# Performance work log

Measured on AMD Instinct MI355X. Metric: run time of the kernel, lower is better.

## Reference

```python
import jax, jax.numpy as jnp
import numpy as np

BN_EPS = 1e-5

def _batchnorm(h, gamma, beta):
    # PyTorch BatchNorm1d in training mode: biased batch statistics over dim 0
    mu = jnp.mean(h, axis=0)
    var = jnp.mean((h - mu) ** 2, axis=0)
    return (h - mu) * jax.lax.rsqrt(var + BN_EPS) * gamma + beta


def setup_inputs() -> dict:
    key = jax.random.key(0)
    ks = jax.random.split(key, 8)
    N, E, D = 50000, 800000, 128
    x = jax.random.normal(ks[0], (N, D), dtype=jnp.float32)
    edge_index = jax.random.randint(ks[1], (2, E), 0, N, dtype=jnp.int64)
    s1 = 1.0 / np.sqrt(D)
    W1 = jax.random.uniform(ks[2], (D, D), jnp.float32, -s1, s1)
    b1 = jax.random.uniform(ks[3], (D,), jnp.float32, -s1, s1)
    W2 = jax.random.uniform(ks[4], (D, D), jnp.float32, -s1, s1)
    b2 = jax.random.uniform(ks[5], (D,), jnp.float32, -s1, s1)
    g1 = jnp.ones((D,), jnp.float32); beta1 = jnp.zeros((D,), jnp.float32)
    g2 = jnp.ones((D,), jnp.float32); beta2 = jnp.zeros((D,), jnp.float32)
    eps = jnp.array([0.1], jnp.float32)
    return {"x": x, "edge_index": edge_index, "eps": eps,
            "W1": W1, "b1": b1, "g1": g1, "beta1": beta1,
            "W2": W2, "b2": b2, "g2": g2, "beta2": beta2}


def reference(x, edge_index, eps, W1, b1, g1, beta1, W2, b2, g2, beta2):
    src, dst = edge_index[0], edge_index[1]
    N = x.shape[0]
    # gather by src, scatter-add to dst
    aggr = jax.ops.segment_sum(x[src], dst, num_segments=N)
    out = (1.0 + eps) * x + aggr  # eps broadcast (shape [1])
    h = jax.nn.relu(_batchnorm(out @ W1 + b1, g1, beta1))
    h = jax.nn.relu(_batchnorm(h @ W2 + b2, g2, beta2))
    return h
```

## Files before the change

kernel.cpp:

```cpp
#include <hip/hip_runtime.h>

#define D 128
#define FB 4096
#define GCAP 1024

typedef __attribute__((ext_vector_type(8))) short short8;
typedef __attribute__((ext_vector_type(4))) float f32x4;

static __device__ __forceinline__ unsigned short f2bf(float f) {
    union { float f; unsigned u; } v; v.f = f;
    unsigned r = v.u + 0x7FFF + ((v.u >> 16) & 1);
    return (unsigned short)(r >> 16);
}

static __device__ __forceinline__ float2 bfpair2f(unsigned p) {
    union { unsigned u; float f; } a, b;
    a.u = (p & 0xFFFFu) << 16;
    b.u = p & 0xFFFF0000u;
    return make_float2(a.f, b.f);
}

__global__ __launch_bounds__(256) void prep_kernel(
    const float4* __restrict__ x4, uint2* __restrict__ xh, int xtotal,
    const float* __restrict__ W1, const float* __restrict__ W2,
    unsigned short* __restrict__ Wf1, unsigned short* __restrict__ Wf2,
    float* __restrict__ stats, int* __restrict__ bucketCount,
    unsigned short* __restrict__ zrow, int xblocks)
{
    if (blockIdx.x < (unsigned)xblocks) {
        int i = blockIdx.x * 256 + threadIdx.x;
        if (i >= xtotal) return;
        float4 v = x4[i];
        uint2 o;
        o.x = (unsigned)f2bf(v.x) | ((unsigned)f2bf(v.y) << 16);
        o.y = (unsigned)f2bf(v.z) | ((unsigned)f2bf(v.w) << 16);
        xh[i] = o;
    } else if (blockIdx.x < (unsigned)(xblocks + 128)) {
        int idx = (blockIdx.x - xblocks) * 256 + threadIdx.x;
        const float* W = (idx < 16384) ? W1 : W2;
        unsigned short* Wf = (idx < 16384) ? Wf1 : Wf2;
        int e = idx & 16383;
        int j = e & 7, lane = (e >> 3) & 63, ckk = e >> 9;
        int ct = ckk & 7, kk = ckk >> 3;
        int k = kk * 32 + (lane >> 4) * 8 + j;
        int n = ct * 16 + (lane & 15);
        Wf[e] = f2bf(W[k * 128 + n]);
    } else {
        int t = threadIdx.x;
        stats[t] = 0.f; stats[t + 256] = 0.f;
        bucketCount[t] = 0; bucketCount[t + 256] = 0;
        if (t < 128) zrow[t] = 0;
    }
}

__global__ __launch_bounds__(256) void bucket_hist_kernel(
    const int* __restrict__ ei, int E, int NB, int* __restrict__ bucketCount)
{
    __shared__ int hist[512];
    int tid = threadIdx.x;
    for (int i = tid; i < NB; i += 256) hist[i] = 0;
    __syncthreads();
    int b0 = blockIdx.x * FB;
    int lim = min(FB, E - b0);
    for (int i = tid; i < lim; i += 256)
        atomicAdd(&hist[ei[E + b0 + i] >> 7], 1);
    __syncthreads();
    for (int i = tid; i < NB; i += 256)
        if (hist[i]) atomicAdd(&bucketCount[i], hist[i]);
}

__global__ __launch_bounds__(512) void bucket_scan_kernel(
    const int* __restrict__ bucketCount, int NB, int E,
    int* __restrict__ bucketBase, int* __restrict__ bucketCursor)
{
    __shared__ int sm[512];
    int tid = threadIdx.x;
    int v = (tid < NB) ? bucketCount[tid] : 0;
    sm[tid] = v;
    __syncthreads();
    #pragma unroll
    for (int off = 1; off < 512; off <<= 1) {
        int u = (tid >= off) ? sm[tid - off] : 0;
        __syncthreads();
        sm[tid] += u;
        __syncthreads();
    }
    if (tid < NB) {
        int ex = sm[tid] - v;
        bucketBase[tid] = ex;
        bucketCursor[tid] = ex;
    }
    if (tid == 0) bucketBase[NB] = E;
}

__global__ __launch_bounds__(256) void bucket_fill_kernel(
    const int* __restrict__ ei, int E, int NB,
    int* __restrict__ bucketCursor, unsigned* __restrict__ rec)
{
    __shared__ int hist[512], base[512];
    int tid = threadIdx.x;
    int b0 = blockIdx.x * FB;
    for (int i = tid; i < NB; i += 256) hist[i] = 0;
    __syncthreads();
    int lim = min(FB, E - b0);
    for (int i = tid; i < lim; i += 256)
        atomicAdd(&hist[ei[E + b0 + i] >> 7], 1);
    __syncthreads();
    for (int i = tid; i < NB; i += 256) {
        int c = hist[i];
        base[i] = c ? atomicAdd(&bucketCursor[i], c) : 0;
        hist[i] = 0;
    }
    __syncthreads();
    for (int i = tid; i < lim; i += 256) {
        int e = b0 + i;
        int dst = ei[E + e], src = ei[e];
        int bk = dst >> 7;
        int r = atomicAdd(&hist[bk], 1);
        rec[base[bk] + r] = ((unsigned)src << 7) | (unsigned)(dst & 127);
    }
}

__global__ __launch_bounds__(256) void bucket_gather_kernel(
    const unsigned* __restrict__ xh, const unsigned* __restrict__ rec,
    const int* __restrict__ bucketBase, const float* __restrict__ epsp,
    unsigned* __restrict__ h0, int N, int zrow)
{
    int bk = blockIdx.x >> 2;
    int sub = blockIdx.x & 3;
    int tid = threadIdx.x;
    int d0 = (bk << 7) + (sub << 5);

    __shared__ int cnts[32], rnk[32], offs[33];
    __shared__ int slist[GCAP];

    if (tid < 32) { cnts[tid] = 0; rnk[tid] = 0; }
    __syncthreads();

    int lo = bucketBase[bk], hi = bucketBase[bk + 1];
    for (int i = lo + tid; i < hi; i += 256) {
        unsigned r = rec[i];
        int dl = r & 127;
        if ((dl >> 5) == sub) atomicAdd(&cnts[dl & 31], 1);
    }
    __syncthreads();
    if (tid == 0) {
        int run = 0;
        #pragma unroll
        for (int i = 0; i < 32; ++i) { offs[i] = run; run += cnts[i]; }
        offs[32] = run;
    }
    __syncthreads();
    for (int i = lo + tid; i < hi; i += 256) {
        unsigned r = rec[i];
        int dl = r & 127;
        if ((dl >> 5) == sub) {
            int d5 = dl & 31;
            int rk = atomicAdd(&rnk[d5], 1);
            int pos = offs[d5] + rk;
            if (pos < GCAP) slist[pos] = (int)(r >> 7);
        }
    }
    __syncthreads();

    int wv = tid >> 6, lane = tid & 63;
    float epsv = 1.0f + __ldg(epsp);

    #pragma unroll 1
    for (int jj = 0; jj < 4; ++jj) {
        int dA = d0 + wv * 8 + jj * 2;
        int dB = dA + 1;
        int vA = (dA < N), vB = (dB < N);
        int iA = offs[(dA - d0)];
        int eA = offs[(dA - d0) + 1];
        int iB = vB ? offs[(dB - d0)] : 0;
        int eB = vB ? offs[(dB - d0) + 1] : 0;
        if (iA > GCAP) iA = GCAP;
        if (eA > GCAP) eA = GCAP;
        if (iB > GCAP) iB = GCAP;
        if (eB > GCAP) eB = GCAP;
        if (!vA) { iA = 0; eA = 0; }

        float2 xvA = bfpair2f(xh[(size_t)(vA ? dA : 0) * 64 + lane]);
        float2 xvB = bfpair2f(xh[(size_t)(vB ? dB : 0) * 64 + lane]);
        float axA = epsv * xvA.x, ayA = epsv * xvA.y;
        float axB = epsv * xvB.x, ayB = epsv * xvB.y;

        int iters = (eA - iA) > (eB - iB) ? (eA - iA) : (eB - iB);
        for (int it = 0; it < iters; it += 8) {
            unsigned pvA[8], pvB[8];
            #pragma unroll
            for (int k = 0; k < 8; ++k) {
                int idxA = (iA + k < eA) ? slist[iA + k] : zrow;
                int idxB = (iB + k < eB) ? slist[iB + k] : zrow;
                pvA[k] = xh[(size_t)idxA * 64 + lane];
                pvB[k] = xh[(size_t)idxB * 64 + lane];
            }
            #pragma unroll
            for (int k = 0; k < 8; ++k) {
                float2 a = bfpair2f(pvA[k]);
                float2 b = bfpair2f(pvB[k]);
                axA += a.x; ayA += a.y;
                axB += b.x; ayB += b.y;
            }
            iA += 8; iB += 8;
        }
        if (vA) h0[(size_t)dA * 64 + lane] =
            (unsigned)f2bf(axA) | ((unsigned)f2bf(ayA) << 16);
        if (vB) h0[(size_t)dB * 64 + lane] =
            (unsigned)f2bf(axB) | ((unsigned)f2bf(ayB) << 16);
    }
}

__global__ __launch_bounds__(256) void gemm_bn_mfma_kernel(
    const unsigned short* __restrict__ a_bf,
    const float* __restrict__ stat_in, const float* __restrict__ gamma,
    const float* __restrict__ beta, float invN,
    const unsigned short* __restrict__ Wf, const float* __restrict__ bias,
    unsigned short* __restrict__ zout,
    float* __restrict__ stat_sum, float* __restrict__ stat_sq,
    int N, int mode)
{
    __shared__ unsigned short Wl[16384];
    __shared__ float part[1024];
    __shared__ float scf[128], shf[128];

    int tid = threadIdx.x;
    {
        float4* dst = (float4*)Wl;
        const float4* srcp = (const float4*)Wf;
        #pragma unroll
        for (int i = 0; i < 8; ++i) dst[tid + i * 256] = srcp[tid + i * 256];
    }
    if (mode == 1 && tid < 128) {
        float mean = stat_in[tid] * invN;
        float var  = stat_in[128 + tid] * invN - mean * mean;
        float sv = gamma[tid] * rsqrtf(var + 1e-5f);
        scf[tid] = sv;
        shf[tid] = fmaf(-mean, sv, beta[tid]);
    }
    __syncthreads();

    int w = tid >> 6, lane = tid & 63, q = lane >> 4, n16 = lane & 15;
    int rowb = blockIdx.x * 64 + w * 16;
    int m = rowb + n16;
    int mc = (m < N) ? m : (N - 1);
    const unsigned short* arow = a_bf + (size_t)mc * D;

    f32x4 acc[8];
    #pragma unroll
    for (int ct = 0; ct < 8; ++ct) acc[ct] = (f32x4){0.f, 0.f, 0.f, 0.f};

    #pragma unroll
    for (int kk = 0; kk < 4; ++kk) {
        int c = kk * 32 + q * 8;
        short8 af;
        if (mode == 0) {
            af = *(const short8*)(arow + c);
        } else {
            uint4 rw = *(const uint4*)(arow + c);
            float2 p0 = bfpair2f(rw.x), p1 = bfpair2f(rw.y);
            float2 p2 = bfpair2f(rw.z), p3 = bfpair2f(rw.w);
            p0.x = fmaxf(fmaf(p0.x, scf[c + 0], shf[c + 0]), 0.f);
            p0.y = fmaxf(fmaf(p0.y, scf[c + 1], shf[c + 1]), 0.f);
            p1.x = fmaxf(fmaf(p1.x, scf[c + 2], shf[c + 2]), 0.f);
            p1.y = fmaxf(fmaf(p1.y, scf[c + 3], shf[c + 3]), 0.f);
            p2.x = fmaxf(fmaf(p2.x, scf[c + 4], shf[c + 4]), 0.f);
            p2.y = fmaxf(fmaf(p2.y, scf[c + 5], shf[c + 5]), 0.f);
            p3.x = fmaxf(fmaf(p3.x, scf[c + 6], shf[c + 6]), 0.f);
            p3.y = fmaxf(fmaf(p3.y, scf[c + 7], shf[c + 7]), 0.f);
            af[0] = (short)f2bf(p0.x); af[1] = (short)f2bf(p0.y);
            af[2] = (short)f2bf(p1.x); af[3] = (short)f2bf(p1.y);
            af[4] = (short)f2bf(p2.x); af[5] = (short)f2bf(p2.y);
            af[6] = (short)f2bf(p3.x); af[7] = (short)f2bf(p3.y);
        }
        #pragma unroll
        for (int ct = 0; ct < 8; ++ct) {
            short8 bf = *(const short8*)&Wl[(((kk * 8 + ct) * 64) + lane) * 8];
            acc[ct] = __builtin_amdgcn_mfma_f32_16x16x32_bf16(af, bf, acc[ct], 0, 0, 0);
        }
    }

    #pragma unroll
    for (int ct = 0; ct < 8; ++ct) {
        int col = ct * 16 + n16;
        float bv = __ldg(bias + col);
        float s = 0.f, qs = 0.f;
        #pragma unroll
        for (int reg = 0; reg < 4; ++reg) {
            int row = rowb + q * 4 + reg;
            float v = acc[ct][reg] + bv;
            if (row < N) {
                zout[(size_t)row * D + col] = f2bf(v);
                s += v;
                qs = fmaf(v, v, qs);
            }
        }
        s  += __shfl_xor(s, 16, 64);
        s  += __shfl_xor(s, 32, 64);
        qs += __shfl_xor(qs, 16, 64);
        qs += __shfl_xor(qs, 32, 64);
        if (lane < 16) {
            part[w * 128 + col] = s;
            part[512 + w * 128 + col] = qs;
        }
    }
    __syncthreads();

    if (tid < 128) {
        float s  = part[tid] + part[128 + tid] + part[256 + tid] + part[384 + tid];
        float qq = part[512 + tid] + part[640 + tid] + part[768 + tid] + part[896 + tid];
        atomicAdd(&stat_sum[tid], s);
        atomicAdd(&stat_sq[tid], qq);
    }
}

__global__ __launch_bounds__(256) void bn_relu_kernel(
    const uint2* __restrict__ z2, float4* __restrict__ out,
    const float* __restrict__ stat2, const float* __restrict__ gamma,
    const float* __restrict__ beta, float invN, int total4)
{
    __shared__ float sf[128], tf[128];
    int tid = threadIdx.x;
    if (tid < 128) {
        float mean = stat2[tid] * invN;
        float var  = stat2[128 + tid] * invN - mean * mean;
        float sv = gamma[tid] * rsqrtf(var + 1e-5f);
        sf[tid] = sv;
        tf[tid] = fmaf(-mean, sv, beta[tid]);
    }
    __syncthreads();

    int i = blockIdx.x * 256 + tid;
    if (i >= total4) return;
    uint2 zp = z2[i];
    float2 v01 = bfpair2f(zp.x);
    float2 v23 = bfpair2f(zp.y);
    int c = (i & 31) * 4;
    float4 o;
    o.x = fmaxf(fmaf(v01.x, sf[c + 0], tf[c + 0]), 0.f);
    o.y = fmaxf(fmaf(v01.y, sf[c + 1], tf[c + 1]), 0.f);
    o.z = fmaxf(fmaf(v23.x, sf[c + 2], tf[c + 2]), 0.f);
    o.w = fmaxf(fmaf(v23.y, sf[c + 3], tf[c + 3]), 0.f);
    out[i] = o;
}

extern "C" void kernel_launch(void* const* d_in, const int* in_sizes, int n_in,
                              void* d_out, int out_size, void* d_ws, size_t ws_size,
                              hipStream_t stream)
{
    const float* x   = (const float*)d_in[0];
    const int*   ei  = (const int*)d_in[1];
    const float* eps = (const float*)d_in[2];
    const float* W1  = (const float*)d_in[3];
    const float* b1  = (const float*)d_in[4];
    const float* g1  = (const float*)d_in[5];
    const float* be1 = (const float*)d_in[6];
    const float* W2  = (const float*)d_in[7];
    const float* b2  = (const float*)d_in[8];
    const float* g2  = (const float*)d_in[9];
    const float* be2 = (const float*)d_in[10];

    int N = in_sizes[0] / D;
    int E = in_sizes[1] / 2;
    size_t ND = (size_t)N * D;
    int NB = (N + 127) >> 7;

    unsigned short* xh  = (unsigned short*)d_ws;
    unsigned short* z1  = xh;
    unsigned short* region2 = xh + ND + 128;
    unsigned* rec       = (unsigned*)region2;
    unsigned short* z2  = region2;
    float* stats        = (float*)(region2 + ND);
    int* bucketCount    = (int*)(stats + 512);
    int* bucketBase     = bucketCount + 512;
    int* bucketCursor   = bucketBase + 513;
    unsigned short* Wf1 = (unsigned short*)(bucketCursor + 512);
    unsigned short* Wf2 = Wf1 + 16384;

    float* sum1 = stats + 0,   *sq1 = stats + 128;
    float* sum2 = stats + 256, *sq2 = stats + 384;
    unsigned short* h0 = (unsigned short*)d_out;

    int xtotal = N * 32;
    int xblocks = (xtotal + 255) / 256;
    prep_kernel<<<xblocks + 129, 256, 0, stream>>>(
        (const float4*)x, (uint2*)xh, xtotal, W1, W2, Wf1, Wf2,
        stats, bucketCount, xh + ND, xblocks);

    int fblocks = (E + FB - 1) / FB;
    bucket_hist_kernel<<<fblocks, 256, 0, stream>>>(ei, E, NB, bucketCount);
    bucket_scan_kernel<<<1, 512, 0, stream>>>(bucketCount, NB, E, bucketBase, bucketCursor);
    bucket_fill_kernel<<<fblocks, 256, 0, stream>>>(ei, E, NB, bucketCursor, rec);
    bucket_gather_kernel<<<NB * 4, 256, 0, stream>>>(
        (const unsigned*)xh, rec, bucketBase, eps, (unsigned*)h0, N, N);

    int gblocks = (N + 63) / 64;
    gemm_bn_mfma_kernel<<<gblocks, 256, 0, stream>>>(
        h0, nullptr, nullptr, nullptr, 0.f,
        Wf1, b1, z1, sum1, sq1, N, 0);
    gemm_bn_mfma_kernel<<<gblocks, 256, 0, stream>>>(
        z1, sum1, g1, be1, 1.0f / N,
        Wf2, b2, z2, sum2, sq2, N, 1);
    bn_relu_kernel<<<(N * 32 + 255) / 256, 256, 0, stream>>>(
        (const uint2*)z2, (float4*)d_out, sum2, g2, be2, 1.0f / N, N * 32);
}
```

Baseline: 228.7 us.

## Fuse both GEMM+BatchNorm stages and final ReLU into one kernel with grid barriers

After: 414.6 us. 81.3% more time.

```diff
diff --git a/kernel.cpp b/kernel.cpp
--- a/kernel.cpp
+++ b/kernel.cpp
@@ -20,12 +20,28 @@
     return make_float2(a.f, b.f);
 }
 
+static __device__ __forceinline__ void grid_barrier(int* cnt, int* flag, int nblocks) {
+    __syncthreads();
+    if (threadIdx.x == 0) {
+        __threadfence();
+        int prev = __hip_atomic_fetch_add(cnt, 1, __ATOMIC_ACQ_REL, __HIP_MEMORY_SCOPE_AGENT);
+        if (prev == nblocks - 1) {
+            __hip_atomic_store(flag, 1, __ATOMIC_RELEASE, __HIP_MEMORY_SCOPE_AGENT);
+        } else {
+            while (__hip_atomic_load(flag, __ATOMIC_ACQUIRE, __HIP_MEMORY_SCOPE_AGENT) == 0)
+                __builtin_amdgcn_s_sleep(8);
+        }
+        __threadfence();
+    }
+    __syncthreads();
+}
+
 __global__ __launch_bounds__(256) void prep_kernel(
     const float4* __restrict__ x4, uint2* __restrict__ xh, int xtotal,
     const float* __restrict__ W1, const float* __restrict__ W2,
     unsigned short* __restrict__ Wf1, unsigned short* __restrict__ Wf2,
     float* __restrict__ stats, int* __restrict__ bucketCount,
-    unsigned short* __restrict__ zrow, int xblocks)
+    int* __restrict__ bar, unsigned short* __restrict__ zrow, int xblocks)
 {
     if (blockIdx.x < (unsigned)xblocks) {
         int i = blockIdx.x * 256 + threadIdx.x;
@@ -50,6 +66,7 @@
         stats[t] = 0.f; stats[t + 256] = 0.f;
         bucketCount[t] = 0; bucketCount[t + 256] = 0;
         if (t < 128) zrow[t] = 0;
+        if (t < 4) bar[t] = 0;
     }
 }
 
@@ -212,137 +229,162 @@
     }
 }
 
-__global__ __launch_bounds__(256) void gemm_bn_mfma_kernel(
-    const unsigned short* __restrict__ a_bf,
-    const float* __restrict__ stat_in, const float* __restrict__ gamma,
-    const float* __restrict__ beta, float invN,
-    const unsigned short* __restrict__ Wf, const float* __restrict__ bias,
-    unsigned short* __restrict__ zout,
-    float* __restrict__ stat_sum, float* __restrict__ stat_sq,
-    int N, int mode)
+__global__ __launch_bounds__(256, 4) void mlp_fused_kernel(
+    const unsigned short* h0,
+    const unsigned short* __restrict__ Wf1, const unsigned short* __restrict__ Wf2,
+    const float* __restrict__ b1, const float* __restrict__ g1, const float* __restrict__ be1,
+    const float* __restrict__ b2, const float* __restrict__ g2, const float* __restrict__ be2,
+    float* __restrict__ stats, int* __restrict__ bar,
+    float* out, int N, int nblocks, float invN)
 {
     __shared__ unsigned short Wl[16384];
-    __shared__ float part[1024];
+    __shared__ char ubuf[5120];
     __shared__ float scf[128], shf[128];
+    float* part = (float*)ubuf;
+    unsigned short* trans = (unsigned short*)ubuf;
 
     int tid = threadIdx.x;
-    {
-        float4* dst = (float4*)Wl;
-        const float4* srcp = (const float4*)Wf;
-        #pragma unroll
-        for (int i = 0; i < 8; ++i) dst[tid + i * 256] = srcp[tid + i * 256];
-    }
-    if (mode == 1 && tid < 128) {
-        float mean = stat_in[tid] * invN;
-        float var  = stat_in[128 + tid] * invN - mean * mean;
-        float sv = gamma[tid] * rsqrtf(var + 1e-5f);
-        scf[tid] = sv;
-        shf[tid] = fmaf(-mean, sv, beta[tid]);
-    }
-    __syncthreads();
-
     int w = tid >> 6, lane = tid & 63, q = lane >> 4, n16 = lane & 15;
     int rowb = blockIdx.x * 64 + w * 16;
     int m = rowb + n16;
     int mc = (m < N) ? m : (N - 1);
-    const unsigned short* arow = a_bf + (size_t)mc * D;
-
-    f32x4 acc[8];
+
+    {
+        float4* dst = (float4*)Wl;
+        const float4* srcp = (const float4*)Wf1;
+        #pragma unroll
+        for (int i = 0; i < 8; ++i) dst[tid + i * 256] = srcp[tid + i * 256];
+    }
+    __syncthreads();
+
+    const unsigned short* arow = h0 + (size_t)mc * D;
+    f32x4 acc[8], acc2[8];
     #pragma unroll
     for (int ct = 0; ct < 8; ++ct) acc[ct] = (f32x4){0.f, 0.f, 0.f, 0.f};
-
     #pragma unroll
     for (int kk = 0; kk < 4; ++kk) {
-        int c = kk * 32 + q * 8;
-        short8 af;
-        if (mode == 0) {
-            af = *(const short8*)(arow + c);
-        } else {
-            uint4 rw = *(const uint4*)(arow + c);
-            float2 p0 = bfpair2f(rw.x), p1 = bfpair2f(rw.y);
-            float2 p2 = bfpair2f(rw.z), p3 = bfpair2f(rw.w);
-            p0.x = fmaxf(fmaf(p0.x, scf[c + 0], shf[c + 0]), 0.f);
-            p0.y = fmaxf(fmaf(p0.y, scf[c + 1], shf[c + 1]), 0.f);
-            p1.x = fmaxf(fmaf(p1.x, scf[c + 2], shf[c + 2]), 0.f);
-            p1.y = fmaxf(fmaf(p1.y, scf[c + 3], shf[c + 3]), 0.f);
-            p2.x = fmaxf(fmaf(p2.x, scf[c + 4], shf[c + 4]), 0.f);
-            p2.y = fmaxf(fmaf(p2.y, scf[c + 5], shf[c + 5]), 0.f);
-            p3.x = fmaxf(fmaf(p3.x, scf[c + 6], shf[c + 6]), 0.f);
-            p3.y = fmaxf(fmaf(p3.y, scf[c + 7], shf[c + 7]), 0.f);
-            af[0] = (short)f2bf(p0.x); af[1] = (short)f2bf(p0.y);
-            af[2] = (short)f2bf(p1.x); af[3] = (short)f2bf(p1.y);
-            af[4] = (short)f2bf(p2.x); af[5] = (short)f2bf(p2.y);
-            af[6] = (short)f2bf(p3.x); af[7] = (short)f2bf(p3.y);
-        }
+        short8 af = *(const short8*)(arow + kk * 32 + q * 8);
         #pragma unroll
         for (int ct = 0; ct < 8; ++ct) {
             short8 bf = *(const short8*)&Wl[(((kk * 8 + ct) * 64) + lane) * 8];
             acc[ct] = __builtin_amdgcn_mfma_f32_16x16x32_bf16(af, bf, acc[ct], 0, 0, 0);
         }
     }
-
     #pragma unroll
     for (int ct = 0; ct < 8; ++ct) {
         int col = ct * 16 + n16;
-        float bv = __ldg(bias + col);
+        float bv = __ldg(b1 + col);
         float s = 0.f, qs = 0.f;
         #pragma unroll
         for (int reg = 0; reg < 4; ++reg) {
             int row = rowb + q * 4 + reg;
             float v = acc[ct][reg] + bv;
-            if (row < N) {
-                zout[(size_t)row * D + col] = f2bf(v);
-                s += v;
-                qs = fmaf(v, v, qs);
-            }
-        }
-        s  += __shfl_xor(s, 16, 64);
-        s  += __shfl_xor(s, 32, 64);
-        qs += __shfl_xor(qs, 16, 64);
-        qs += __shfl_xor(qs, 32, 64);
-        if (lane < 16) {
-            part[w * 128 + col] = s;
-            part[512 + w * 128 + col] = qs;
-        }
-    }
-    __syncthreads();
-
+            acc[ct][reg] = v;
+            if (row < N) { s += v; qs = fmaf(v, v, qs); }
+        }
+        s  += __shfl_xor(s, 16, 64);  s  += __shfl_xor(s, 32, 64);
+        qs += __shfl_xor(qs, 16, 64); qs += __shfl_xor(qs, 32, 64);
+        if (lane < 16) { part[w * 128 + col] = s; part[512 + w * 128 + col] = qs; }
+    }
+    __syncthreads();
     if (tid < 128) {
         float s  = part[tid] + part[128 + tid] + part[256 + tid] + part[384 + tid];
         float qq = part[512 + tid] + part[640 + tid] + part[768 + tid] + part[896 + tid];
-        atomicAdd(&stat_sum[tid], s);
-        atomicAdd(&stat_sq[tid], qq);
-    }
-}
-
-__global__ __launch_bounds__(256) void bn_relu_kernel(
-    const uint2* __restrict__ z2, float4* __restrict__ out,
-    const float* __restrict__ stat2, const float* __restrict__ gamma,
-    const float* __restrict__ beta, float invN, int total4)
-{
-    __shared__ float sf[128], tf[128];
-    int tid = threadIdx.x;
+        atomicAdd(&stats[tid], s);
+        atomicAdd(&stats[128 + tid], qq);
+    }
+
+    grid_barrier(&bar[0], &bar[1], nblocks);
+
     if (tid < 128) {
-        float mean = stat2[tid] * invN;
-        float var  = stat2[128 + tid] * invN - mean * mean;
-        float sv = gamma[tid] * rsqrtf(var + 1e-5f);
-        sf[tid] = sv;
-        tf[tid] = fmaf(-mean, sv, beta[tid]);
-    }
-    __syncthreads();
-
-    int i = blockIdx.x * 256 + tid;
-    if (i >= total4) return;
-    uint2 zp = z2[i];
-    float2 v01 = bfpair2f(zp.x);
-    float2 v23 = bfpair2f(zp.y);
-    int c = (i & 31) * 4;
-    float4 o;
-    o.x = fmaxf(fmaf(v01.x, sf[c + 0], tf[c + 0]), 0.f);
-    o.y = fmaxf(fmaf(v01.y, sf[c + 1], tf[c + 1]), 0.f);
-    o.z = fmaxf(fmaf(v23.x, sf[c + 2], tf[c + 2]), 0.f);
-    o.w = fmaxf(fmaf(v23.y, sf[c + 3], tf[c + 3]), 0.f);
-    out[i] = o;
+        float sm = __hip_atomic_load(&stats[tid], __ATOMIC_RELAXED, __HIP_MEMORY_SCOPE_AGENT);
+        float sq = __hip_atomic_load(&stats[128 + tid], __ATOMIC_RELAXED, __HIP_MEMORY_SCOPE_AGENT);
+        float mean = sm * invN;
+        float var  = sq * invN - mean * mean;
+        float sv = __ldg(g1 + tid) * rsqrtf(var + 1e-5f);
+        scf[tid] = sv;
+        shf[tid] = fmaf(-mean, sv, __ldg(be1 + tid));
+    }
+    {
+        float4* dst = (float4*)Wl;
+        const float4* srcp = (const float4*)Wf2;
+        #pragma unroll
+        for (int i = 0; i < 8; ++i) dst[tid + i * 256] = srcp[tid + i * 256];
+    }
+    __syncthreads();
+
+    #pragma unroll
+    for (int ct = 0; ct < 8; ++ct) acc2[ct] = (f32x4){0.f, 0.f, 0.f, 0.f};
+    unsigned short* tw = trans + w * 640;
+    #pragma unroll
+    for (int kk = 0; kk < 4; ++kk) {
+        #pragma unroll
+        for (int ct2 = 0; ct2 < 2; ++ct2) {
+            int ct = kk * 2 + ct2;
+            int col = ct * 16 + n16;
+            float sc_ = scf[col], sh_ = shf[col];
+            #pragma unroll
+            for (int reg = 0; reg < 4; ++reg) {
+                float v = fmaxf(fmaf(acc[ct][reg], sc_, sh_), 0.f);
+                tw[(q * 4 + reg) * 40 + ct2 * 16 + n16] = f2bf(v);
+            }
+        }
+        __syncthreads();
+        short8 af = *(const short8*)&tw[n16 * 40 + q * 8];
+        #pragma unroll
+        for (int cto = 0; cto < 8; ++cto) {
+            short8 bf = *(const short8*)&Wl[(((kk * 8 + cto) * 64) + lane) * 8];
+            acc2[cto] = __builtin_amdgcn_mfma_f32_16x16x32_bf16(af, bf, acc2[cto], 0, 0, 0);
+        }
+        __syncthreads();
+    }
+    #pragma unroll
+    for (int ct = 0; ct < 8; ++ct) {
+        int col = ct * 16 + n16;
+        float bv = __ldg(b2 + col);
+        float s = 0.f, qs = 0.f;
+        #pragma unroll
+        for (int reg = 0; reg < 4; ++reg) {
+            int row = rowb + q * 4 + reg;
+            float v = acc2[ct][reg] + bv;
+            acc2[ct][reg] = v;
+            if (row < N) { s += v; qs = fmaf(v, v, qs); }
+        }
+        s  += __shfl_xor(s, 16, 64);  s  += __shfl_xor(s, 32, 64);
+        qs += __shfl_xor(qs, 16, 64); qs += __shfl_xor(qs, 32, 64);
+        if (lane < 16) { part[w * 128 + col] = s; part[512 + w * 128 + col] = qs; }
+    }
+    __syncthreads();
+    if (tid < 128) {
+        float s  = part[tid] + part[128 + tid] + part[256 + tid] + part[384 + tid];
+        float qq = part[512 + tid] + part[640 + tid] + part[768 + tid] + part[896 + tid];
+        atomicAdd(&stats[256 + tid], s);
+        atomicAdd(&stats[384 + tid], qq);
+    }
+
+    grid_barrier(&bar[2], &bar[3], nblocks);
+
+    if (tid < 128) {
+        float sm = __hip_atomic_load(&stats[256 + tid], __ATOMIC_RELAXED, __HIP_MEMORY_SCOPE_AGENT);
+        float sq = __hip_atomic_load(&stats[384 + tid], __ATOMIC_RELAXED, __HIP_MEMORY_SCOPE_AGENT);
+        float mean = sm * invN;
+        float var  = sq * invN - mean * mean;
+        float sv = __ldg(g2 + tid) * rsqrtf(var + 1e-5f);
+        scf[tid] = sv;
+        shf[tid] = fmaf(-mean, sv, __ldg(be2 + tid));
+    }
+    __syncthreads();
+    #pragma unroll
+    for (int ct = 0; ct < 8; ++ct) {
+        int col = ct * 16 + n16;
+        float sc_ = scf[col], sh_ = shf[col];
+        #pragma unroll
+        for (int reg = 0; reg < 4; ++reg) {
+            int row = rowb + q * 4 + reg;
+            if (row < N)
+                out[(size_t)row * D + col] = fmaxf(fmaf(acc2[ct][reg], sc_, sh_), 0.f);
+        }
+    }
 }
 
 extern "C" void kernel_launch(void* const* d_in, const int* in_sizes, int n_in,
@@ -367,26 +409,23 @@
     int NB = (N + 127) >> 7;
 
     unsigned short* xh  = (unsigned short*)d_ws;
-    unsigned short* z1  = xh;
     unsigned short* region2 = xh + ND + 128;
     unsigned* rec       = (unsigned*)region2;
-    unsigned short* z2  = region2;
     float* stats        = (float*)(region2 + ND);
     int* bucketCount    = (int*)(stats + 512);
     int* bucketBase     = bucketCount + 512;
     int* bucketCursor   = bucketBase + 513;
-    unsigned short* Wf1 = (unsigned short*)(bucketCursor + 512);
+    int* bar            = bucketCursor + 512;
+    unsigned short* Wf1 = (unsigned short*)(bar + 4);
     unsigned short* Wf2 = Wf1 + 16384;
 
-    float* sum1 = stats + 0,   *sq1 = stats + 128;
-    float* sum2 = stats + 256, *sq2 = stats + 384;
     unsigned short* h0 = (unsigned short*)d_out;
 
     int xtotal = N * 32;
     int xblocks = (xtotal + 255) / 256;
     prep_kernel<<<xblocks + 129, 256, 0, stream>>>(
         (const float4*)x, (uint2*)xh, xtotal, W1, W2, Wf1, Wf2,
-        stats, bucketCount, xh + ND, xblocks);
+        stats, bucketCount, bar, xh + ND, xblocks);
 
     int fblocks = (E + FB - 1) / FB;
     bucket_hist_kernel<<<fblocks, 256, 0, stream>>>(ei, E, NB, bucketCount);
@@ -396,12 +435,7 @@
         (const unsigned*)xh, rec, bucketBase, eps, (unsigned*)h0, N, N);
 
     int gblocks = (N + 63) / 64;
-    gemm_bn_mfma_kernel<<<gblocks, 256, 0, stream>>>(
-        h0, nullptr, nullptr, nullptr, 0.f,
-        Wf1, b1, z1, sum1, sq1, N, 0);
-    gemm_bn_mfma_kernel<<<gblocks, 256, 0, stream>>>(
-        z1, sum1, g1, be1, 1.0f / N,
-        Wf2, b2, z2, sum2, sq2, N, 1);
-    bn_relu_kernel<<<(N * 32 + 255) / 256, 256, 0, stream>>>(
-        (const uint2*)z2, (float4*)d_out, sum2, g2, be2, 1.0f / N, N * 32);
-}
+    mlp_fused_kernel<<<gblocks, 256, 0, stream>>>(
+        h0, Wf1, Wf2, b1, g1, be1, b2, g2, be2,
+        stats, bar, (float*)d_out, N, gblocks, 1.0f / N);
+}
```
